# Kernel optimization log

Measured on AMD Instinct MI355X. Metric: run time of the kernel, lower is better.

The kernel has to match this reference:

```python
import jax, jax.numpy as jnp
import numpy as np

K = 1024  # num_points to sample (matches init_kwargs)


def setup_inputs() -> dict:
    key = jax.random.key(0)
    k1, k2 = jax.random.split(key)
    B, N, C = 16, 100000, 16
    points = jax.random.normal(k1, (B, N, C), dtype=jnp.float32)
    start_idx = jax.random.randint(k2, (B,), 0, N, dtype=jnp.int32)
    return {"points": points, "start_idx": start_idx}


def _sample_farthest_points(xyz, start_idx, k):
    # xyz: [B, N, 3], start_idx: [B] int32. Returns idx: [B, k] int32.
    B, N, _ = xyz.shape

    def body(carry, _):
        min_d, last = carry                                    # [B,N], [B]
        sel = jnp.take_along_axis(xyz, last[:, None, None], axis=1)  # [B,1,3]
        d = jnp.sum((xyz - sel) ** 2, axis=-1)                 # [B,N]
        min_d = jnp.minimum(min_d, d)
        nxt = jnp.argmax(min_d, axis=-1).astype(jnp.int32)     # [B]
        return (min_d, nxt), last

    init = (jnp.full((B, N), jnp.inf, dtype=xyz.dtype), start_idx)
    _, idx = jax.lax.scan(body, init, None, length=k)          # idx: [k, B]
    return idx.T                                               # [B, k]


def reference(points, start_idx):
    # Faithful 'fps' strategy: farthest point sampling on xyz, gather all channels.
    xyz = points[:, :, :3].astype(jnp.float32)
    idx = _sample_farthest_points(xyz, start_idx, K)           # [B, K]
    out = jnp.take_along_axis(points, idx[:, :, None], axis=1) # [B, K, C]
    return out
```

## Files before the change

### kernel.cpp

```cpp
#include <hip/hip_runtime.h>

#define NB    16
#define NPTS  100000
#define NCH   16
#define KSEL  1024
#define SLOTS 8
#define TPB   256
#define CHUNK 12500
#define PPT   49
#define MAGA  0x19u
#define MAGB  0x13u

typedef unsigned long long u64;
typedef unsigned int u32;


__device__ __forceinline__ void combine(float ov, int oi, float& v, int& i) {
  if (ov > v || (ov == v && oi < i)) { v = ov; i = oi; }
}

__global__ __launch_bounds__(TPB, 1)
void fps_kernel(const float* __restrict__ points, const int* __restrict__ start_idx,
                u64* __restrict__ ws_cand, int* __restrict__ ws_idx) {
  const int raw  = blockIdx.x;
  const int b    = raw >> 3;
  const int slot = raw & 7;

  const int tid  = threadIdx.x;
  const int lane = tid & 63;
  const int wid  = tid >> 6;

  const int base = slot * CHUNK;
  const float* __restrict__ pb = points + (size_t)b * NPTS * NCH;

  float px[PPT], py[PPT], pz[PPT], md[PPT];
  #pragma unroll
  for (int k = 0; k < PPT; ++k) {
    const int li = tid + (k << 8);
    const bool valid = li < CHUNK;
    float4 p = make_float4(0.f, 0.f, 0.f, 0.f);
    if (valid) p = *reinterpret_cast<const float4*>(pb + (size_t)(base + li) * NCH);
    px[k] = p.x; py[k] = p.y; pz[k] = p.z;
    md[k] = valid ? __builtin_inff() : -__builtin_inff();
  }
  #pragma unroll
  for (int k = 0; k < PPT; ++k)
    asm volatile("" : "+v"(px[k]), "+v"(py[k]), "+v"(pz[k]), "+v"(md[k]));

  __shared__ float s_rv[4];
  __shared__ int   s_ri[4];
  __shared__ float s_wx, s_wy, s_wz;

  const int sidx = start_idx[b];
  float sx, sy, sz;
  {
    const float4 p = *reinterpret_cast<const float4*>(pb + (size_t)sidx * NCH);
    sx = p.x; sy = p.y; sz = p.z;
  }
  if (slot == 0 && tid == 0) ws_idx[b * KSEL] = sidx;

  for (int i = 0; i < KSEL - 1; ++i) {
    const int par = i & 1;
    u64* const blk = ws_cand + (((size_t)par * NB + b) << 5);

    float bv = -__builtin_inff();
    int   bi = 0x7fffffff;
    #pragma unroll
    for (int k = 0; k < PPT; ++k) {
      const float dx = __fsub_rn(px[k], sx);
      const float dy = __fsub_rn(py[k], sy);
      const float dz = __fsub_rn(pz[k], sz);
      const float d  = __fadd_rn(__fadd_rn(__fmul_rn(dx, dx), __fmul_rn(dy, dy)),
                                 __fmul_rn(dz, dz));
      const float m  = fminf(md[k], d);
      md[k] = m;
      if (m > bv) { bv = m; bi = base + tid + (k << 8); }
    }

    #pragma unroll
    for (int m = 32; m >= 1; m >>= 1) {
      const float ov = __shfl_xor(bv, m, 64);
      const int   oi = __shfl_xor(bi, m, 64);
      combine(ov, oi, bv, bi);
    }
    if (lane == 0) { s_rv[wid] = bv; s_ri[wid] = bi; }
    __syncthreads();

    bv = s_rv[0]; bi = s_ri[0];
    #pragma unroll
    for (int w = 1; w < 4; ++w) combine(s_rv[w], s_ri[w], bv, bi);

    const u32 tm = (u32)(i + 1) << 5;

    const int local = bi - base;
    if (tid == (local & 255)) {
      const int kk = local >> 8;
      float ox = 0.f, oy = 0.f, oz = 0.f;
      #pragma unroll
      for (int k = 0; k < PPT; ++k)
        if (k == kk) { ox = px[k]; oy = py[k]; oz = pz[k]; }
      const u32 inv = 131071u - (u32)bi;
      const u32 loA = (inv << 15) | tm | MAGA;
      const u32 loB = (inv << 15) | tm | MAGB;
      __hip_atomic_store(blk      + slot, ((u64)__float_as_uint(bv) << 32) | loA,
                         __ATOMIC_RELAXED, __HIP_MEMORY_SCOPE_AGENT);
      __hip_atomic_store(blk +  8 + slot, ((u64)__float_as_uint(ox) << 32) | loB,
                         __ATOMIC_RELAXED, __HIP_MEMORY_SCOPE_AGENT);
      __hip_atomic_store(blk + 16 + slot, ((u64)__float_as_uint(oy) << 32) | loB,
                         __ATOMIC_RELAXED, __HIP_MEMORY_SCOPE_AGENT);
      __hip_atomic_store(blk + 24 + slot, ((u64)__float_as_uint(oz) << 32) | loB,
                         __ATOMIC_RELAXED, __HIP_MEMORY_SCOPE_AGENT);
    }

    if (wid == 0) {
      const bool active = lane < 32;
      const int  word   = lane >> 3;
      const u32  want   = tm | (word == 0 ? MAGA : MAGB);
      u64 q = 0;
      for (;;) {
        if (active) q = __hip_atomic_load(blk + lane, __ATOMIC_RELAXED, __HIP_MEMORY_SCOPE_AGENT);
        if (__all(!active || (((u32)q & 0x7FFFu) == want))) break;
        __builtin_amdgcn_s_sleep(1);
      }
      u64 key = (active && word == 0) ? q : 0;
      #pragma unroll
      for (int m = 4; m >= 1; m >>= 1) {
        const u64 o = __shfl_xor(key, m, 64);
        if (o > key) key = o;
      }
      const u64 kmax = __shfl(key, 0, 64);
      const unsigned long long ball = __ballot(active && word == 0 && q == kmax);
      const int ws = __ffsll(ball) - 1;
      const u32 hi = (u32)(q >> 32);
      const u32 xb = (u32)__shfl((int)hi,  8 + ws, 64);
      const u32 yb = (u32)__shfl((int)hi, 16 + ws, 64);
      const u32 zb = (u32)__shfl((int)hi, 24 + ws, 64);
      if (lane == 0) {
        s_wx = __uint_as_float(xb);
        s_wy = __uint_as_float(yb);
        s_wz = __uint_as_float(zb);
        if (slot == 0)
          ws_idx[b * KSEL + i + 1] = 131071 - (int)((kmax >> 15) & 0x1FFFFu);
      }
    }
    __syncthreads();
    sx = s_wx; sy = s_wy; sz = s_wz;
  }
}

__global__ void gather_kernel(const float* __restrict__ points,
                              const int* __restrict__ ws_idx,
                              float* __restrict__ out) {
  const int e = blockIdx.x * 256 + threadIdx.x;
  const int c = e & 15;
  const int k = (e >> 4) & (KSEL - 1);
  const int b = e >> 14;
  const int idx = ws_idx[b * KSEL + k];
  out[e] = points[((size_t)b * NPTS + idx) * NCH + c];
}

extern "C" void kernel_launch(void* const* d_in, const int* in_sizes, int n_in,
                              void* d_out, int out_size, void* d_ws, size_t ws_size,
                              hipStream_t stream) {
  const float* points    = (const float*)d_in[0];
  const int*   start_idx = (const int*)d_in[1];
  float*       out       = (float*)d_out;

  u64* cand = (u64*)((char*)d_ws + 4096);
  int* idxl = (int*)((char*)d_ws + 65536);

  hipMemsetAsync(cand, 0, 2 * NB * 4 * SLOTS * sizeof(u64), stream);

  fps_kernel<<<NB * SLOTS, TPB, 0, stream>>>(points, start_idx, cand, idxl);
  gather_kernel<<<(NB * KSEL * NCH) / 256, 256, 0, stream>>>(points, idxl, out);
}
```

Before: 3.527 ms.

## Double slots per batch with XCD-local block placement and L2 fast-path exchange

Splits each batch across 16 blocks instead of 8, halving points per thread, and fills all 256 CUs. Each block reads its hardware XCC id and claims a (batch, slot) assignment so that the 16 blocks of one batch tend to sit on the same XCD. The per-iteration candidate exchange now writes to an L2-local fast buffer, polled with sc0 loads, alongside a device-scope slow buffer that serves as a fallback. The goal is lower cross-block synchronization latency per iteration, at the cost of more participants in each exchange and extra stores.

```diff
diff --git a/kernel.cpp b/kernel.cpp
--- a/kernel.cpp
+++ b/kernel.cpp
@@ -4,10 +4,10 @@
 #define NPTS  100000
 #define NCH   16
 #define KSEL  1024
-#define SLOTS 8
+#define SLOTS 16
 #define TPB   256
-#define CHUNK 12500
-#define PPT   49
+#define CHUNK 6250
+#define PPT   25
 #define MAGA  0x19u
 #define MAGB  0x13u
 
@@ -19,16 +19,49 @@
   if (ov > v || (ov == v && oi < i)) { v = ov; i = oi; }
 }
 
+__device__ __forceinline__ void st_l2(u64* p, u64 v) {
+  asm volatile("global_store_dwordx2 %0, %1, off" :: "v"(p), "v"(v) : "memory");
+}
+__device__ __forceinline__ u64 ld_sc0(const u64* p) {
+  u64 r;
+  asm volatile("global_load_dwordx2 %0, %1, off sc0\n\ts_waitcnt vmcnt(0)"
+               : "=v"(r) : "v"(p) : "memory");
+  return r;
+}
+
 __global__ __launch_bounds__(TPB, 1)
 void fps_kernel(const float* __restrict__ points, const int* __restrict__ start_idx,
-                u64* __restrict__ ws_cand, int* __restrict__ ws_idx) {
-  const int raw  = blockIdx.x;
-  const int b    = raw >> 3;
-  const int slot = raw & 7;
-
+                int* __restrict__ ws_cnt, int* __restrict__ ws_claim,
+                u64* __restrict__ ws_fast, u64* __restrict__ ws_slow,
+                int* __restrict__ ws_idx) {
   const int tid  = threadIdx.x;
   const int lane = tid & 63;
   const int wid  = tid >> 6;
+
+  __shared__ int s_bs;
+  if (tid == 0) {
+    u32 xcd;
+    asm volatile("s_getreg_b32 %0, hwreg(HW_REG_XCC_ID, 0, 32)" : "=s"(xcd));
+    xcd &= 7u;
+    const int rank = __hip_atomic_fetch_add(ws_cnt + xcd, 1, __ATOMIC_RELAXED,
+                                            __HIP_MEMORY_SCOPE_AGENT);
+    const int pref = (rank < 32) ? ((int)xcd * 32 + rank) : -1;
+    int got = -1;
+    if (pref >= 0 &&
+        __hip_atomic_exchange(ws_claim + pref, 1, __ATOMIC_RELAXED,
+                              __HIP_MEMORY_SCOPE_AGENT) == 0)
+      got = pref;
+    for (int j = 0; got < 0 && j < 512; ++j) {
+      const int idx = ((pref >= 0 ? pref + 1 : 0) + j) & 255;
+      if (__hip_atomic_exchange(ws_claim + idx, 1, __ATOMIC_RELAXED,
+                                __HIP_MEMORY_SCOPE_AGENT) == 0)
+        got = idx;
+    }
+    s_bs = got;
+  }
+  __syncthreads();
+  const int b    = s_bs >> 4;
+  const int slot = s_bs & 15;
 
   const int base = slot * CHUNK;
   const float* __restrict__ pb = points + (size_t)b * NPTS * NCH;
@@ -61,7 +94,8 @@
 
   for (int i = 0; i < KSEL - 1; ++i) {
     const int par = i & 1;
-    u64* const blk = ws_cand + (((size_t)par * NB + b) << 5);
+    u64* const fblk = ws_fast + (((size_t)par * NB + b) << 6);
+    u64* const sblk = ws_slow + (((size_t)par * NB + b) << 6);
 
     float bv = -__builtin_inff();
     int   bi = 0x7fffffff;
@@ -100,41 +134,52 @@
       for (int k = 0; k < PPT; ++k)
         if (k == kk) { ox = px[k]; oy = py[k]; oz = pz[k]; }
       const u32 inv = 131071u - (u32)bi;
-      const u32 loA = (inv << 15) | tm | MAGA;
-      const u32 loB = (inv << 15) | tm | MAGB;
-      __hip_atomic_store(blk      + slot, ((u64)__float_as_uint(bv) << 32) | loA,
-                         __ATOMIC_RELAXED, __HIP_MEMORY_SCOPE_AGENT);
-      __hip_atomic_store(blk +  8 + slot, ((u64)__float_as_uint(ox) << 32) | loB,
-                         __ATOMIC_RELAXED, __HIP_MEMORY_SCOPE_AGENT);
-      __hip_atomic_store(blk + 16 + slot, ((u64)__float_as_uint(oy) << 32) | loB,
-                         __ATOMIC_RELAXED, __HIP_MEMORY_SCOPE_AGENT);
-      __hip_atomic_store(blk + 24 + slot, ((u64)__float_as_uint(oz) << 32) | loB,
-                         __ATOMIC_RELAXED, __HIP_MEMORY_SCOPE_AGENT);
+      const u64 w0 = ((u64)__float_as_uint(bv) << 32) | (inv << 15) | tm | MAGA;
+      const u64 mt = (u64)((inv << 15) | tm | MAGB);
+      const u64 w1 = ((u64)__float_as_uint(ox) << 32) | mt;
+      const u64 w2 = ((u64)__float_as_uint(oy) << 32) | mt;
+      const u64 w3 = ((u64)__float_as_uint(oz) << 32) | mt;
+      st_l2(fblk      + slot, w0);
+      st_l2(fblk + 16 + slot, w1);
+      st_l2(fblk + 32 + slot, w2);
+      st_l2(fblk + 48 + slot, w3);
+      __hip_atomic_store(sblk      + slot, w0, __ATOMIC_RELAXED, __HIP_MEMORY_SCOPE_AGENT);
+      __hip_atomic_store(sblk + 16 + slot, w1, __ATOMIC_RELAXED, __HIP_MEMORY_SCOPE_AGENT);
+      __hip_atomic_store(sblk + 32 + slot, w2, __ATOMIC_RELAXED, __HIP_MEMORY_SCOPE_AGENT);
+      __hip_atomic_store(sblk + 48 + slot, w3, __ATOMIC_RELAXED, __HIP_MEMORY_SCOPE_AGENT);
     }
 
     if (wid == 0) {
-      const bool active = lane < 32;
-      const int  word   = lane >> 3;
-      const u32  want   = tm | (word == 0 ? MAGA : MAGB);
+      const int  word = lane >> 4;
+      const u32  want = tm | (word == 0 ? MAGA : MAGB);
       u64 q = 0;
+      bool got = false;
+      int r = 0;
       for (;;) {
-        if (active) q = __hip_atomic_load(blk + lane, __ATOMIC_RELAXED, __HIP_MEMORY_SCOPE_AGENT);
-        if (__all(!active || (((u32)q & 0x7FFFu) == want))) break;
-        __builtin_amdgcn_s_sleep(1);
+        if (!got) {
+          const u64 t = ld_sc0(fblk + lane);
+          if (((u32)t & 0x7FFFu) == want) { q = t; got = true; }
+        }
+        if (__all(got)) break;
+        if (!got && ((++r & 15) == 0)) {
+          const u64 t = __hip_atomic_load(sblk + lane, __ATOMIC_RELAXED,
+                                          __HIP_MEMORY_SCOPE_AGENT);
+          if (((u32)t & 0x7FFFu) == want) { q = t; got = true; }
+        }
       }
-      u64 key = (active && word == 0) ? q : 0;
+      u64 key = (word == 0) ? q : 0;
       #pragma unroll
-      for (int m = 4; m >= 1; m >>= 1) {
+      for (int m = 8; m >= 1; m >>= 1) {
         const u64 o = __shfl_xor(key, m, 64);
         if (o > key) key = o;
       }
       const u64 kmax = __shfl(key, 0, 64);
-      const unsigned long long ball = __ballot(active && word == 0 && q == kmax);
-      const int ws = __ffsll(ball) - 1;
+      const unsigned long long ball = __ballot(word == 0 && q == kmax);
+      const int rs = __ffsll(ball) - 1;
       const u32 hi = (u32)(q >> 32);
-      const u32 xb = (u32)__shfl((int)hi,  8 + ws, 64);
-      const u32 yb = (u32)__shfl((int)hi, 16 + ws, 64);
-      const u32 zb = (u32)__shfl((int)hi, 24 + ws, 64);
+      const u32 xb = (u32)__shfl((int)hi, 16 + rs, 64);
+      const u32 yb = (u32)__shfl((int)hi, 32 + rs, 64);
+      const u32 zb = (u32)__shfl((int)hi, 48 + rs, 64);
       if (lane == 0) {
         s_wx = __uint_as_float(xb);
         s_wy = __uint_as_float(yb);
@@ -166,11 +211,14 @@
   const int*   start_idx = (const int*)d_in[1];
   float*       out       = (float*)d_out;
 
-  u64* cand = (u64*)((char*)d_ws + 4096);
-  int* idxl = (int*)((char*)d_ws + 65536);
-
-  hipMemsetAsync(cand, 0, 2 * NB * 4 * SLOTS * sizeof(u64), stream);
-
-  fps_kernel<<<NB * SLOTS, TPB, 0, stream>>>(points, start_idx, cand, idxl);
+  int* cnt   = (int*)d_ws;
+  int* claim = (int*)((char*)d_ws + 64);
+  u64* fast  = (u64*)((char*)d_ws + 4096);
+  u64* slow  = (u64*)((char*)d_ws + 20480);
+  int* idxl  = (int*)((char*)d_ws + 65536);
+
+  hipMemsetAsync(d_ws, 0, 36864, stream);
+
+  fps_kernel<<<NB * SLOTS, TPB, 0, stream>>>(points, start_idx, cnt, claim, fast, slow, idxl);
   gather_kernel<<<(NB * KSEL * NCH) / 256, 256, 0, stream>>>(points, idxl, out);
 }
```

New measurement: 4.706 ms. 1.33x slower.
